# Kernel optimization log

Measured on AMD Instinct MI355X. Metric: run time of the kernel, lower is better.

Reference implementation:

```python
import jax, jax.numpy as jnp
import numpy as np

HID = 150

def _lstm_layer(x, Wih, Whh, bih, bhh):
    # x: [T, D] -> [T, HID]; PyTorch gate order i, f, g, o
    b = bih + bhh
    xg = x @ Wih.T + b  # precompute input contribution: [T, 4H]
    def step(carry, xg_t):
        h, c = carry
        g = xg_t + h @ Whh.T
        i, f, gg, o = jnp.split(g, 4)
        i = jax.nn.sigmoid(i); f = jax.nn.sigmoid(f)
        gg = jnp.tanh(gg); o = jax.nn.sigmoid(o)
        c = f * c + i * gg
        h = o * jnp.tanh(c)
        return (h, c), h
    init = (jnp.zeros((HID,), x.dtype), jnp.zeros((HID,), x.dtype))
    _, ys = jax.lax.scan(step, init, xg)
    return ys

def _bilstm(x, Wih, Whh, bih, bhh):
    # x: [T, D]; params stacked [L, 2, ...]
    out = x
    for l in range(Wih.shape[0]):
        fwd = _lstm_layer(out, Wih[l, 0], Whh[l, 0], bih[l, 0], bhh[l, 0])
        bwd = _lstm_layer(out[::-1], Wih[l, 1], Whh[l, 1], bih[l, 1], bhh[l, 1])[::-1]
        out = jnp.concatenate([fwd, bwd], axis=-1)  # [T, 2H]
    return out

def setup_inputs() -> dict:
    key = jax.random.key(0)
    ks = jax.random.split(key, 16)
    s = 0.1  # keep LSTM gates in a sane range
    return {
        "inputs_solv": jax.random.normal(ks[0], (1, 4096, 300), jnp.float32),
        "inputs_solu": jax.random.normal(ks[1], (1, 4096, 300), jnp.float32),
        "solv_Wih": jax.random.normal(ks[2], (2, 2, 600, 300), jnp.float32) * s,
        "solv_Whh": jax.random.normal(ks[3], (2, 2, 600, 150), jnp.float32) * s,
        "solv_bih": jax.random.normal(ks[4], (2, 2, 600), jnp.float32) * s,
        "solv_bhh": jax.random.normal(ks[5], (2, 2, 600), jnp.float32) * s,
        "solu_Wih": jax.random.normal(ks[6], (2, 2, 600, 300), jnp.float32) * s,
        "solu_Whh": jax.random.normal(ks[7], (2, 2, 600, 150), jnp.float32) * s,
        "solu_bih": jax.random.normal(ks[8], (2, 2, 600), jnp.float32) * s,
        "solu_bhh": jax.random.normal(ks[9], (2, 2, 600), jnp.float32) * s,
        "fc1_w": jax.random.normal(ks[10], (2000, 600), jnp.float32) * 0.02,
        "fc1_b": jax.random.normal(ks[11], (2000,), jnp.float32) * 0.02,
        "fc2_w": jax.random.normal(ks[12], (1, 2000), jnp.float32) * 0.02,
        "fc2_b": jax.random.normal(ks[13], (1,), jnp.float32) * 0.02,
    }

def reference(inputs_solv, inputs_solu, solv_Wih, solv_Whh, solv_bih, solv_bhh,
              solu_Wih, solu_Whh, solu_bih, solu_bhh, fc1_w, fc1_b, fc2_w, fc2_b):
    H = _bilstm(inputs_solv[0], solv_Wih, solv_Whh, solv_bih, solv_bhh)  # [Hs, 300]
    G = _bilstm(inputs_solu[0], solu_Wih, solu_Whh, solu_bih, solu_bhh)  # [Gs, 300]
    a_score = H @ G.T                      # fused version of the nested loop: [Hs, Gs]
    a = jax.nn.softmax(a_score, axis=1)
    P = a @ G                              # [Hs, 300]
    Q = a.T @ H                            # [Gs, 300]
    u = jnp.maximum(H, P)
    v = jnp.maximum(G, Q)
    inp = jnp.concatenate([u.sum(axis=0), v.sum(axis=0)], axis=0)  # [600]
    x = jax.nn.relu(inp @ fc1_w.T + fc1_b)
    return x @ fc2_w.T + fc2_b
```

## Files before the change

### kernel.cpp

```cpp
#include <hip/hip_runtime.h>
#include <hip/hip_fp16.h>
#include <cstddef>

#define T_LEN 4096
#define HID 150
#define G4 600
#define NC 300

typedef __attribute__((ext_vector_type(8))) short bf16x8;
typedef __attribute__((ext_vector_type(8))) _Float16 f16x8;
typedef __attribute__((ext_vector_type(4))) float f32x4;

__device__ __forceinline__ void barrier_lgkm() {
  asm volatile("s_waitcnt lgkmcnt(0)\n\ts_barrier" ::: "memory");
}

__device__ __forceinline__ float fsig(float x) {
  return __builtin_amdgcn_rcpf(1.f + __expf(-x));
}
__device__ __forceinline__ float ftanh(float x) {
  float ax = fabsf(x);
  float e = __expf(2.f * ax);
  float t = 1.f - 2.f * __builtin_amdgcn_rcpf(e + 1.f);
  return copysignf(t, x);
}
__device__ __forceinline__ unsigned short f2bf(float f) {
  unsigned u = __builtin_bit_cast(unsigned, f);
  u += 0x7fff + ((u >> 16) & 1);
  return (unsigned short)(u >> 16);
}

template <int W32>
__global__ __launch_bounds__(512, 2) void lstm_scan(
    const float* __restrict__ whh_solv, const float* __restrict__ whh_solu,
    const float* __restrict__ xg_base,
    float* __restrict__ o32v, float* __restrict__ o32u,
    __half* __restrict__ o16v, __half* __restrict__ o16u, int layer)
{
  __shared__ __align__(16) unsigned short h_bf[160];
  __shared__ __align__(16) float g4[160][4];
  const int c = blockIdx.x;
  const int net = c >> 1, dir = c & 1;
  const float* Whh = (net ? whh_solu : whh_solv) + (size_t)(layer * 2 + dir) * (G4 * HID);
  const float* xg = xg_base + (size_t)c * T_LEN * G4;
  float* out32 = (net ? o32u : o32v) + dir * HID;
  __half* out16 = (net ? o16u : o16v) + dir * HID;
  const int tid = threadIdx.x;
  const int lane = tid & 63, wv = tid >> 6;
  const int lrow = lane & 15, lq = lane >> 4;

  bf16x8 bfr[5][5];
#pragma unroll
  for (int j = 0; j < 5; j++) {
    const int T = wv + 8 * j, gt = T & 3, uw = T >> 2;
    const int un = 16 * uw + lrow;
#pragma unroll
    for (int kk = 0; kk < 5; kk++) {
      bf16x8 b;
#pragma unroll
      for (int i = 0; i < 8; i++) {
        const int k = kk * 32 + lq * 8 + i;
        const float v = (un < HID && k < HID) ? Whh[(size_t)(gt * HID + un) * HID + k] : 0.f;
        b[i] = (short)f2bf(v);
      }
      bfr[j][kk] = b;
    }
  }
  if (tid < 160) h_bf[tid] = 0;

  const int t0 = dir ? (T_LEN - 1) : 0;
  const int d16 = dir ? -320 : 320;
  const int d32 = dir ? -NC : NC;
  const int dxg = dir ? -G4 : G4;
  float cst = 0.f;
  float xr0 = 0.f, xr1 = 0.f, xr2 = 0.f, xr3 = 0.f;
  const float* xgp = xg + (size_t)t0 * G4 + tid;
  __half* o16p = out16 + (size_t)t0 * 320 + tid;
  float* o32p = out32 + (size_t)t0 * NC + tid;
  if (tid < HID) { xr0 = xgp[0]; xr1 = xgp[HID]; xr2 = xgp[2 * HID]; xr3 = xgp[3 * HID]; }
  barrier_lgkm();

  for (int s = 0; s < T_LEN; s++) {
    bf16x8 af[5];
#pragma unroll
    for (int kk = 0; kk < 5; kk++) {
      bf16x8 a = {0, 0, 0, 0, 0, 0, 0, 0};
      if (lrow == 0) a = *(const bf16x8*)&h_bf[kk * 32 + lq * 8];
      af[kk] = a;
    }
    f32x4 acc[5];
#pragma unroll
    for (int j = 0; j < 5; j++) acc[j] = (f32x4){0.f, 0.f, 0.f, 0.f};
#pragma unroll
    for (int kk = 0; kk < 5; kk++)
#pragma unroll
      for (int j = 0; j < 5; j++)
        acc[j] = __builtin_amdgcn_mfma_f32_16x16x32_bf16(af[kk], bfr[j][kk], acc[j], 0, 0, 0);
    if (lane < 16) {
      float* g4f = &g4[0][0];
#pragma unroll
      for (int j = 0; j < 5; j++) {
        const int T = wv + 8 * j, gt = T & 3, uw = T >> 2;
        const int u = 16 * uw + lane;
        g4f[4 * u + (gt ^ ((u >> 3) & 3))] = acc[j][0];
      }
    }
    barrier_lgkm();
    if (tid < HID) {
      const f32x4 g = *(const f32x4*)&g4[tid][0];
      const int p = (tid >> 3) & 3;
      const bool p1 = (p & 1) != 0, p2 = (p & 2) != 0;
      const float a0 = p1 ? g[1] : g[0];
      const float a1 = p1 ? g[0] : g[1];
      const float a2 = p1 ? g[3] : g[2];
      const float a3 = p1 ? g[2] : g[3];
      float gi = xr0 + (p2 ? a2 : a0);
      float gf = xr1 + (p2 ? a3 : a1);
      float gg = xr2 + (p2 ? a0 : a2);
      float go = xr3 + (p2 ? a1 : a3);
      xgp += dxg;
      if (s + 1 < T_LEN) {
        xr0 = xgp[0]; xr1 = xgp[HID]; xr2 = xgp[2 * HID]; xr3 = xgp[3 * HID];
      }
      const float iv = fsig(gi), fv = fsig(gf), gv = ftanh(gg), ov = fsig(go);
      cst = fv * cst + iv * gv;
      const float hv = ov * ftanh(cst);
      h_bf[tid] = f2bf(hv);
      *o16p = __float2half(hv);
      o16p += d16;
      if (W32) { *o32p = hv; o32p += d32; }
    }
    barrier_lgkm();
  }
}

__global__ void conv_w(const float* __restrict__ wv, const float* __restrict__ wu,
                       __half* __restrict__ dst, float* __restrict__ inp)
{
  const int gid = blockIdx.x * 256 + threadIdx.x;
  if (gid < 640) inp[gid] = 0.f;
  if (gid >= 8 * 640 * 320) return;
  const int k = gid % 320, j = (gid / 320) % 640, s = gid / (320 * 640);
  const int l = s >> 2, net = (s >> 1) & 1, dir = s & 1;
  float v = 0.f;
  if (j < G4 && k < NC) {
    const float* src = (net ? wu : wv) + (size_t)(l * 2 + dir) * (G4 * NC);
    v = src[(size_t)j * NC + k];
  }
  dst[gid] = __float2half(v);
}

__global__ void conv_x2(const float* __restrict__ s0, const float* __restrict__ s1,
                        __half* __restrict__ d0, __half* __restrict__ d1,
                        __half* __restrict__ z0, __half* __restrict__ z1)
{
  const int gid = blockIdx.x * 256 + threadIdx.x;
  if (gid >= 4096 * 320) return;
  const float* src = blockIdx.y ? s1 : s0;
  __half* dst = blockIdx.y ? d1 : d0;
  __half* zp = blockIdx.y ? z1 : z0;
  zp[gid] = (__half)0.f;
  const int k = gid % 320, m = gid / 320;
  dst[gid] = __float2half(k < NC ? src[(size_t)m * NC + k] : 0.f);
}

__global__ void conv_t2(const float* __restrict__ s0, const float* __restrict__ s1,
                        __half* __restrict__ d0, __half* __restrict__ d1)
{
  const int gid = blockIdx.x * 256 + threadIdx.x;
  if (gid >= 320 * 4096) return;
  const float* src = blockIdx.y ? s1 : s0;
  __half* dst = blockIdx.y ? d1 : d0;
  const int m = gid % 4096, f = gid / 4096;
  dst[gid] = __float2half(f < NC ? src[(size_t)m * NC + f] : 0.f);
}

__global__ __launch_bounds__(256) void xg_mfma(
    const __half* __restrict__ Av, const __half* __restrict__ Au,
    const __half* __restrict__ W,
    const float* __restrict__ bihv, const float* __restrict__ bhhv,
    const float* __restrict__ bihu, const float* __restrict__ bhhu,
    float* __restrict__ xg, int layer)
{
  const int tid = threadIdx.x;
  const int lane = tid & 63, wv = tid >> 6;
  const int ln = lane & 15, q = lane >> 4;
  const int chain = blockIdx.y;
  const __half* A = (chain >= 2) ? Au : Av;
  const __half* Wc = W + (size_t)chain * 640 * 320;
  const float* bi = ((chain >= 2) ? bihu : bihv) + (size_t)(layer * 2 + (chain & 1)) * G4;
  const float* bh = ((chain >= 2) ? bhhu : bhhv) + (size_t)(layer * 2 + (chain & 1)) * G4;
  float* C = xg + (size_t)chain * T_LEN * G4;
  const int m0 = blockIdx.x * 64 + wv * 16;
  const __half* Arow = A + (size_t)(m0 + ln) * 320;

  for (int nc = 0; nc < 4; nc++) {
    f32x4 acc[10];
#pragma unroll
    for (int j = 0; j < 10; j++) acc[j] = (f32x4){0.f, 0.f, 0.f, 0.f};
    for (int kk = 0; kk < 10; kk++) {
      const f16x8 afr = *(const f16x8*)(Arow + kk * 32 + q * 8);
#pragma unroll
      for (int j = 0; j < 10; j++) {
        const int n = nc * 160 + j * 16 + ln;
        const f16x8 bfr = *(const f16x8*)(Wc + (size_t)n * 320 + kk * 32 + q * 8);
        acc[j] = __builtin_amdgcn_mfma_f32_16x16x32_f16(afr, bfr, acc[j], 0, 0, 0);
      }
    }
#pragma unroll
    for (int j = 0; j < 10; j++) {
      const int n = nc * 160 + j * 16 + ln;
      if (n < G4) {
        const float bias = bi[n] + bh[n];
#pragma unroll
        for (int r = 0; r < 4; r++)
          C[(size_t)(m0 + q * 4 + r) * G4 + n] = acc[j][r] + bias;
      }
    }
  }
}

__global__ __launch_bounds__(256) void s_gemm(
    const __half* __restrict__ Hh, const __half* __restrict__ Gh,
    __half* __restrict__ AH)
{
  const int tid = threadIdx.x;
  const int lane = tid & 63, wv = tid >> 6;
  const int ln = lane & 15, q = lane >> 4;
  const int m0 = blockIdx.x * 64 + wv * 16;
  const __half* Arow = Hh + (size_t)(m0 + ln) * 320;
  f16x8 afr[10];
#pragma unroll
  for (int kk = 0; kk < 10; kk++) afr[kk] = *(const f16x8*)(Arow + kk * 32 + q * 8);
  const int nt0 = blockIdx.y * 64;
  for (int nt = 0; nt < 64; nt++) {
    const int n = 16 * (nt0 + nt) + ln;
    const __half* Brow = Gh + (size_t)n * 320;
    f32x4 acc = (f32x4){0.f, 0.f, 0.f, 0.f};
#pragma unroll
    for (int kk = 0; kk < 10; kk++) {
      const f16x8 bfr = *(const f16x8*)(Brow + kk * 32 + q * 8);
      acc = __builtin_amdgcn_mfma_f32_16x16x32_f16(afr[kk], bfr, acc, 0, 0, 0);
    }
#pragma unroll
    for (int r = 0; r < 4; r++)
      AH[(size_t)(m0 + q * 4 + r) * 4096 + n] = __float2half(acc[r]);
  }
}

__global__ __launch_bounds__(256) void softmax_k(__half* __restrict__ AH)
{
  const int m = blockIdx.x, tid = threadIdx.x;
  __half* row = AH + (size_t)m * 4096;
  float e[16];
  float s = 0.f;
#pragma unroll
  for (int c = 0; c < 2; c++) {
    const f16x8 v = *(const f16x8*)(row + c * 2048 + tid * 8);
#pragma unroll
    for (int j = 0; j < 8; j++) {
      const float ev = __expf(fminf((float)v[j] - 30.f, 80.f));
      e[c * 8 + j] = ev;
      s += ev;
    }
  }
#pragma unroll
  for (int off = 32; off > 0; off >>= 1) s += __shfl_down(s, off);
  __shared__ float red[4];
  if ((tid & 63) == 0) red[tid >> 6] = s;
  __syncthreads();
  const float ilm = 1.f / (red[0] + red[1] + red[2] + red[3]);
#pragma unroll
  for (int c = 0; c < 2; c++) {
    f16x8 v;
#pragma unroll
    for (int j = 0; j < 8; j++) v[j] = (_Float16)(e[c * 8 + j] * ilm);
    *(f16x8*)(row + c * 2048 + tid * 8) = v;
  }
}

__global__ __launch_bounds__(256) void pq_mfma(
    const __half* __restrict__ AH, const __half* __restrict__ GhT,
    const __half* __restrict__ HhT,
    float* __restrict__ Pb, float* __restrict__ Qb)
{
  __shared__ __align__(16) _Float16 Ats[64][72];
  const int tid = threadIdx.x;
  const int lane = tid & 63, wv = tid >> 6;
  const int ln = lane & 15, q = lane >> 4;

  if (blockIdx.x < 64) {
    const int m0 = blockIdx.x * 64 + wv * 16;
    const __half* Arow = AH + (size_t)(m0 + ln) * 4096;
    for (int nc = 0; nc < 2; nc++) {
      f32x4 acc[10];
#pragma unroll
      for (int j = 0; j < 10; j++) acc[j] = (f32x4){0.f, 0.f, 0.f, 0.f};
      for (int kk = 0; kk < 128; kk++) {
        const f16x8 afr = *(const f16x8*)(Arow + kk * 32 + q * 8);
#pragma unroll
        for (int j = 0; j < 10; j++) {
          const int n = nc * 160 + j * 16 + ln;
          const f16x8 bfr = *(const f16x8*)(GhT + (size_t)n * 4096 + kk * 32 + q * 8);
          acc[j] = __builtin_amdgcn_mfma_f32_16x16x32_f16(afr, bfr, acc[j], 0, 0, 0);
        }
      }
#pragma unroll
      for (int j = 0; j < 10; j++) {
        const int n = nc * 160 + j * 16 + ln;
        if (n < NC) {
#pragma unroll
          for (int r = 0; r < 4; r++)
            Pb[(size_t)(m0 + q * 4 + r) * NC + n] = acc[j][r];
        }
      }
    }
  } else {
    const int j0 = (blockIdx.x - 64) * 64;
    f32x4 acc[20];
#pragma unroll
    for (int j = 0; j < 20; j++) acc[j] = (f32x4){0.f, 0.f, 0.f, 0.f};
    const int il8 = tid >> 2, j8 = (tid & 3) * 16;
    for (int ic = 0; ic < 4096; ic += 64) {
      __syncthreads();
      {
        const __half* src = AH + (size_t)(ic + il8) * 4096 + j0 + j8;
        const f16x8 v0 = *(const f16x8*)src;
        const f16x8 v1 = *(const f16x8*)(src + 8);
#pragma unroll
        for (int jj = 0; jj < 8; jj++) Ats[j8 + jj][il8] = v0[jj];
#pragma unroll
        for (int jj = 0; jj < 8; jj++) Ats[j8 + 8 + jj][il8] = v1[jj];
      }
      __syncthreads();
#pragma unroll
      for (int s = 0; s < 2; s++) {
        const f16x8 afr = *(const f16x8*)&Ats[wv * 16 + ln][s * 32 + q * 8];
        const __half* bbase = HhT + ic + s * 32 + q * 8;
#pragma unroll
        for (int j = 0; j < 20; j++) {
          const f16x8 bfr = *(const f16x8*)(bbase + (size_t)(j * 16 + ln) * 4096);
          acc[j] = __builtin_amdgcn_mfma_f32_16x16x32_f16(afr, bfr, acc[j], 0, 0, 0);
        }
      }
    }
#pragma unroll
    for (int j = 0; j < 20; j++) {
      const int f = j * 16 + ln;
      if (f < NC) {
#pragma unroll
        for (int r = 0; r < 4; r++)
          Qb[(size_t)(j0 + wv * 16 + q * 4 + r) * NC + f] = acc[j][r];
      }
    }
  }
}

__global__ void reduce_uv2(const float* __restrict__ Hb, const float* __restrict__ Pb,
                           const float* __restrict__ Gb, const float* __restrict__ Qb,
                           float* __restrict__ inp)
{
  const int j = threadIdx.x;
  if (j >= NC) return;
  const float* X = blockIdx.y ? Gb : Hb;
  const float* Yp = blockIdx.y ? Qb : Pb;
  const int off = blockIdx.y ? NC : 0;
  const int r0 = blockIdx.x * 128;
  float s = 0.f;
  for (int r = r0; r < r0 + 128; r++)
    s += fmaxf(X[(size_t)r * NC + j], Yp[(size_t)r * NC + j]);
  atomicAdd(&inp[off + j], s);
}

__global__ __launch_bounds__(256) void fc1_k(
    const float* __restrict__ w1, const float* __restrict__ b1,
    const float* __restrict__ inp, float* __restrict__ x)
{
  const int r = blockIdx.x * 4 + (threadIdx.x >> 6);
  const int lane = threadIdx.x & 63;
  const float* wr = w1 + (size_t)r * 600;
  float s = 0.f;
  for (int k = lane; k < 600; k += 64) s += wr[k] * inp[k];
#pragma unroll
  for (int off = 32; off > 0; off >>= 1) s += __shfl_down(s, off);
  if (lane == 0) x[r] = fmaxf(s + b1[r], 0.f);
}

__global__ void fc2_k(const float* __restrict__ x, const float* __restrict__ w2,
                      const float* __restrict__ b2, float* __restrict__ outp)
{
  const int tid = threadIdx.x;
  float s = 0.f;
  for (int i = tid; i < 2000; i += 256) s += x[i] * w2[i];
#pragma unroll
  for (int off = 32; off > 0; off >>= 1) s += __shfl_down(s, off);
  __shared__ float red[4];
  if ((tid & 63) == 0) red[tid >> 6] = s;
  __syncthreads();
  if (tid == 0) outp[0] = red[0] + red[1] + red[2] + red[3] + b2[0];
}

extern "C" void kernel_launch(void* const* d_in, const int* in_sizes, int n_in,
                              void* d_out, int out_size, void* d_ws, size_t ws_size,
                              hipStream_t stream)
{
  const float* in_solv  = (const float*)d_in[0];
  const float* in_solu  = (const float*)d_in[1];
  const float* solv_Wih = (const float*)d_in[2];
  const float* solv_Whh = (const float*)d_in[3];
  const float* solv_bih = (const float*)d_in[4];
  const float* solv_bhh = (const float*)d_in[5];
  const float* solu_Wih = (const float*)d_in[6];
  const float* solu_Whh = (const float*)d_in[7];
  const float* solu_bih = (const float*)d_in[8];
  const float* solu_bhh = (const float*)d_in[9];
  const float* fc1_w = (const float*)d_in[10];
  const float* fc1_b = (const float*)d_in[11];
  const float* fc2_w = (const float*)d_in[12];
  const float* fc2_b = (const float*)d_in[13];
  float* outp = (float*)d_out;
  float* ws = (float*)d_ws;

  constexpr size_t off_P   = 0;
  constexpr size_t off_Q   = 1228800;
  constexpr size_t off_inp = 2457600;
  constexpr size_t off_x   = 2458240;
  constexpr size_t off_xg  = 2468480;
  constexpr size_t off_L0  = off_xg + (size_t)4 * 2457600;
  constexpr size_t off_HG  = off_L0 + 1310720;

  float*  xg   = ws + off_xg;
  float*  Hb   = ws + off_HG;
  float*  Gb   = Hb + 1228800;
  float*  Pb   = ws + off_P;
  float*  Qb   = ws + off_Q;
  float*  inp  = ws + off_inp;
  float*  xf   = ws + off_x;
  __half* Wihh = (__half*)(ws + off_P);
  __half* Avh  = (__half*)(ws + off_L0);
  __half* Auh  = Avh + 4096 * 320;
  __half* L0vh = (__half*)(ws + off_HG);
  __half* L0uh = L0vh + 4096 * 320;
  __half* Hh   = (__half*)(ws + off_L0);
  __half* Gh   = Hh + 4096 * 320;
  __half* AH   = (__half*)(ws + off_xg);
  __half* HhT  = AH + (size_t)4096 * 4096;
  __half* GhT  = HhT + 320 * 4096;

  conv_w<<<(8 * 640 * 320 + 255) / 256, 256, 0, stream>>>(solv_Wih, solu_Wih, Wihh, inp);
  conv_x2<<<dim3(5120, 2), 256, 0, stream>>>(in_solv, in_solu, Avh, Auh, L0vh, L0uh);

  xg_mfma<<<dim3(64, 4), 256, 0, stream>>>(Avh, Auh, Wihh,
      solv_bih, solv_bhh, solu_bih, solu_bhh, xg, 0);
  lstm_scan<0><<<4, 512, 0, stream>>>(solv_Whh, solu_Whh, xg,
      nullptr, nullptr, L0vh, L0uh, 0);

  xg_mfma<<<dim3(64, 4), 256, 0, stream>>>(L0vh, L0uh, Wihh + (size_t)4 * 640 * 320,
      solv_bih, solv_bhh, solu_bih, solu_bhh, xg, 1);
  lstm_scan<1><<<4, 512, 0, stream>>>(solv_Whh, solu_Whh, xg,
      Hb, Gb, Hh, Gh, 1);

  conv_t2<<<dim3(5120, 2), 256, 0, stream>>>(Hb, Gb, HhT, GhT);
  s_gemm<<<dim3(64, 4), 256, 0, stream>>>(Hh, Gh, AH);
  softmax_k<<<4096, 256, 0, stream>>>(AH);
  pq_mfma<<<128, 256, 0, stream>>>(AH, GhT, HhT, Pb, Qb);

  reduce_uv2<<<dim3(32, 2), 320, 0, stream>>>(Hb, Pb, Gb, Qb, inp);
  fc1_k<<<500, 256, 0, stream>>>(fc1_w, fc1_b, inp, xf);
  fc2_k<<<1, 256, 0, stream>>>(xf, fc2_w, fc2_b, outp);
}
```

Baseline: 7.073 ms.

## Fuse max-sum reduction into PQ GEMM epilogue and simplify gate staging

The separate reduce_uv2 kernel is removed. The PQ GEMM epilogue now computes max(H,P) and max(G,Q), reduces them across lanes with shuffles, and atomically accumulates into the input vector, so the P and Q buffers are never written to or read back from global memory. conv_t2 now reads the half-precision H/G copies instead of the fp32 buffers. The LSTM scan drops its XOR-swizzled gate staging layout for a plain indexed layout, which removes select logic but may add LDS bank conflicts on the serial critical path.

```diff
diff --git a/kernel.cpp b/kernel.cpp
--- a/kernel.cpp
+++ b/kernel.cpp
@@ -97,27 +97,19 @@
       for (int j = 0; j < 5; j++)
         acc[j] = __builtin_amdgcn_mfma_f32_16x16x32_bf16(af[kk], bfr[j][kk], acc[j], 0, 0, 0);
     if (lane < 16) {
-      float* g4f = &g4[0][0];
 #pragma unroll
       for (int j = 0; j < 5; j++) {
         const int T = wv + 8 * j, gt = T & 3, uw = T >> 2;
-        const int u = 16 * uw + lane;
-        g4f[4 * u + (gt ^ ((u >> 3) & 3))] = acc[j][0];
+        g4[16 * uw + lane][gt] = acc[j][0];
       }
     }
     barrier_lgkm();
     if (tid < HID) {
       const f32x4 g = *(const f32x4*)&g4[tid][0];
-      const int p = (tid >> 3) & 3;
-      const bool p1 = (p & 1) != 0, p2 = (p & 2) != 0;
-      const float a0 = p1 ? g[1] : g[0];
-      const float a1 = p1 ? g[0] : g[1];
-      const float a2 = p1 ? g[3] : g[2];
-      const float a3 = p1 ? g[2] : g[3];
-      float gi = xr0 + (p2 ? a2 : a0);
-      float gf = xr1 + (p2 ? a3 : a1);
-      float gg = xr2 + (p2 ? a0 : a2);
-      float go = xr3 + (p2 ? a1 : a3);
+      float gi = xr0 + g[0];
+      float gf = xr1 + g[1];
+      float gg = xr2 + g[2];
+      float go = xr3 + g[3];
       xgp += dxg;
       if (s + 1 < T_LEN) {
         xr0 = xgp[0]; xr1 = xgp[HID]; xr2 = xgp[2 * HID]; xr3 = xgp[3 * HID];
@@ -164,15 +156,15 @@
   dst[gid] = __float2half(k < NC ? src[(size_t)m * NC + k] : 0.f);
 }
 
-__global__ void conv_t2(const float* __restrict__ s0, const float* __restrict__ s1,
+__global__ void conv_t2(const __half* __restrict__ s0, const __half* __restrict__ s1,
                         __half* __restrict__ d0, __half* __restrict__ d1)
 {
   const int gid = blockIdx.x * 256 + threadIdx.x;
   if (gid >= 320 * 4096) return;
-  const float* src = blockIdx.y ? s1 : s0;
+  const __half* src = blockIdx.y ? s1 : s0;
   __half* dst = blockIdx.y ? d1 : d0;
   const int m = gid % 4096, f = gid / 4096;
-  dst[gid] = __float2half(f < NC ? src[(size_t)m * NC + f] : 0.f);
+  dst[gid] = (f < NC) ? src[(size_t)m * 320 + f] : (__half)0.f;
 }
 
 __global__ __launch_bounds__(256) void xg_mfma(
@@ -279,10 +271,11 @@
   }
 }
 
-__global__ __launch_bounds__(256) void pq_mfma(
+__global__ __launch_bounds__(256) void pq_red(
     const __half* __restrict__ AH, const __half* __restrict__ GhT,
     const __half* __restrict__ HhT,
-    float* __restrict__ Pb, float* __restrict__ Qb)
+    const float* __restrict__ Hb, const float* __restrict__ Gb,
+    float* __restrict__ inp)
 {
   __shared__ __align__(16) _Float16 Ats[64][72];
   const int tid = threadIdx.x;
@@ -309,9 +302,13 @@
       for (int j = 0; j < 10; j++) {
         const int n = nc * 160 + j * 16 + ln;
         if (n < NC) {
+          float sum = 0.f;
 #pragma unroll
           for (int r = 0; r < 4; r++)
-            Pb[(size_t)(m0 + q * 4 + r) * NC + n] = acc[j][r];
+            sum += fmaxf(Hb[(size_t)(m0 + q * 4 + r) * NC + n], acc[j][r]);
+          sum += __shfl_xor(sum, 16);
+          sum += __shfl_xor(sum, 32);
+          if (q == 0) atomicAdd(&inp[n], sum);
         }
       }
     }
@@ -348,28 +345,16 @@
     for (int j = 0; j < 20; j++) {
       const int f = j * 16 + ln;
       if (f < NC) {
+        float sum = 0.f;
 #pragma unroll
         for (int r = 0; r < 4; r++)
-          Qb[(size_t)(j0 + wv * 16 + q * 4 + r) * NC + f] = acc[j][r];
-      }
-    }
-  }
-}
-
-__global__ void reduce_uv2(const float* __restrict__ Hb, const float* __restrict__ Pb,
-                           const float* __restrict__ Gb, const float* __restrict__ Qb,
-                           float* __restrict__ inp)
-{
-  const int j = threadIdx.x;
-  if (j >= NC) return;
-  const float* X = blockIdx.y ? Gb : Hb;
-  const float* Yp = blockIdx.y ? Qb : Pb;
-  const int off = blockIdx.y ? NC : 0;
-  const int r0 = blockIdx.x * 128;
-  float s = 0.f;
-  for (int r = r0; r < r0 + 128; r++)
-    s += fmaxf(X[(size_t)r * NC + j], Yp[(size_t)r * NC + j]);
-  atomicAdd(&inp[off + j], s);
+          sum += fmaxf(Gb[(size_t)(j0 + wv * 16 + q * 4 + r) * NC + f], acc[j][r]);
+        sum += __shfl_xor(sum, 16);
+        sum += __shfl_xor(sum, 32);
+        if (q == 0) atomicAdd(&inp[NC + f], sum);
+      }
+    }
+  }
 }
 
 __global__ __launch_bounds__(256) void fc1_k(
@@ -422,7 +407,6 @@
   float* ws = (float*)d_ws;
 
   constexpr size_t off_P   = 0;
-  constexpr size_t off_Q   = 1228800;
   constexpr size_t off_inp = 2457600;
   constexpr size_t off_x   = 2458240;
   constexpr size_t off_xg  = 2468480;
@@ -432,8 +416,6 @@
   float*  xg   = ws + off_xg;
   float*  Hb   = ws + off_HG;
   float*  Gb   = Hb + 1228800;
-  float*  Pb   = ws + off_P;
-  float*  Qb   = ws + off_Q;
   float*  inp  = ws + off_inp;
   float*  xf   = ws + off_x;
   __half* Wihh = (__half*)(ws + off_P);
@@ -460,12 +442,11 @@
   lstm_scan<1><<<4, 512, 0, stream>>>(solv_Whh, solu_Whh, xg,
       Hb, Gb, Hh, Gh, 1);
 
-  conv_t2<<<dim3(5120, 2), 256, 0, stream>>>(Hb, Gb, HhT, GhT);
+  conv_t2<<<dim3(5120, 2), 256, 0, stream>>>(Hh, Gh, HhT, GhT);
   s_gemm<<<dim3(64, 4), 256, 0, stream>>>(Hh, Gh, AH);
   softmax_k<<<4096, 256, 0, stream>>>(AH);
-  pq_mfma<<<128, 256, 0, stream>>>(AH, GhT, HhT, Pb, Qb);
-
-  reduce_uv2<<<dim3(32, 2), 320, 0, stream>>>(Hb, Pb, Gb, Qb, inp);
+  pq_red<<<128, 256, 0, stream>>>(AH, GhT, HhT, Hb, Gb, inp);
+
   fc1_k<<<500, 256, 0, stream>>>(fc1_w, fc1_b, inp, xf);
   fc2_k<<<1, 256, 0, stream>>>(xf, fc2_w, fc2_b, outp);
 }
```

New measurement: 6.997 ms (median of 3 runs). About the same (-1.1%).
